# Kernel optimization log

Measured on AMD Instinct MI355X. Metric: run time of the kernel, lower is better.

The kernel has to match this reference:

```python
import jax, jax.numpy as jnp
import numpy as np

B, PP, LP, H = 128, 1024, 128, 256  # graphs, protein atoms/graph, ligand atoms/graph, hidden
NP, NL = B * PP, B * LP


def setup_inputs() -> dict:
    key = jax.random.key(0)
    ks = jax.random.split(key, 16)
    s = 0.02
    return {
        "protein_pos": 10.0 * jax.random.normal(ks[0], (NP, 3), jnp.float32),
        "ligand_pos": 10.0 * jax.random.normal(ks[1], (NL, 3), jnp.float32),
        "protein_element": jax.random.randint(ks[2], (NP,), 0, 128),
        "protein_aa": jax.random.randint(ks[3], (NP,), 0, 32),
        "protein_is_backbone": jax.random.randint(ks[4], (NP,), 0, 2),
        "ligand_type": jax.random.randint(ks[5], (NL,), 0, 16),
        "protein_batch": jnp.repeat(jnp.arange(B), PP),  # block-contiguous segments
        "ligand_batch": jnp.repeat(jnp.arange(B), LP),
        "E_elem": s * jax.random.normal(ks[6], (128, H), jnp.float32),
        "E_aa": s * jax.random.normal(ks[7], (32, H), jnp.float32),
        "E_bb": s * jax.random.normal(ks[8], (2, H), jnp.float32),
        "E_lig": s * jax.random.normal(ks[9], (16, H), jnp.float32),
        "Wd1": s * jax.random.normal(ks[10], (H, H), jnp.float32),
        "bd1": jnp.zeros((H,), jnp.float32),
        "Wd2": s * jax.random.normal(ks[11], (H, H), jnp.float32),
        "bd2": jnp.zeros((H,), jnp.float32),
        "Wa1": s * jax.random.normal(ks[12], (2 * H + 2, H), jnp.float32),
        "ba1": jnp.zeros((H,), jnp.float32),
        "Wa2": s * jax.random.normal(ks[13], (H, 1), jnp.float32),
        "ba2": jnp.zeros((1,), jnp.float32),
    }


def _pool_by_batch(x, batch, bsz):
    # mean-pool rows of x into bsz segments (index_add_ + bincount in torch)
    summed = jax.ops.segment_sum(x, batch, num_segments=bsz)
    counts = jax.ops.segment_sum(jnp.ones((x.shape[0],), x.dtype), batch, num_segments=bsz)
    return summed / jnp.maximum(counts, 1.0)[:, None]


def reference(protein_pos, ligand_pos, protein_element, protein_aa, protein_is_backbone,
              ligand_type, protein_batch, ligand_batch,
              E_elem, E_aa, E_bb, E_lig, Wd1, bd1, Wd2, bd2, Wa1, ba1, Wa2, ba2):
    # protein / ligand node embeddings
    h_protein = E_elem[protein_element] + E_aa[protein_aa] + E_bb[protein_is_backbone]
    h_ligand = E_lig[ligand_type]

    # compose_context: protein first, then ligand (mask_ligand = [0]*NP + [1]*NL)
    h_ctx = jnp.concatenate([h_protein, h_ligand], axis=0)

    # stub denoiser: pointwise 2-layer SiLU MLP producing out['h']
    h_out = jax.nn.silu(h_ctx @ Wd1 + bd1) @ Wd2 + bd2
    protein_h = h_out[:protein_pos.shape[0]]
    ligand_h = h_out[protein_pos.shape[0]:]

    pooled_protein = _pool_by_batch(protein_h, protein_batch, B)  # [B, H]
    pooled_ligand = _pool_by_batch(ligand_h, ligand_batch, B)     # [B, H]

    # contact features: per-graph cdist(lig, prot), min over protein atoms,
    # then mean & min over ligand atoms. Uniform block layout -> dense reshape.
    prot = protein_pos.reshape(B, PP, 3)
    lig = ligand_pos.reshape(B, LP, 3)
    d2 = jnp.sum((lig[:, :, None, :] - prot[:, None, :, :]) ** 2, axis=-1)  # [B, LP, PP]
    dist = jnp.sqrt(d2)
    min_lp = dist.min(axis=2)                                    # [B, LP]
    contact = jnp.stack([min_lp.mean(axis=1), min_lp.min(axis=1)], axis=-1)  # [B, 2]

    graph_feat = jnp.concatenate([pooled_protein, pooled_ligand, contact], axis=-1)  # [B, 2H+2]
    affinity = (jax.nn.silu(graph_feat @ Wa1 + ba1) @ Wa2 + ba2).squeeze(-1)  # [B]
    return affinity
```

## Files before the change

### kernel.cpp

```cpp
#include <hip/hip_runtime.h>
#include <hip/hip_bf16.h>

typedef _Float16 f16;
typedef _Float16 h4 __attribute__((ext_vector_type(4)));
typedef float f32x4 __attribute__((ext_vector_type(4)));

#define B_   128
#define PP_  1024
#define LP_  128
#define H_   256
#define NP_  131072
#define NL_  16384


__global__ void __launch_bounds__(256) prep_k(
    const float* __restrict__ W1,
    const float* __restrict__ Ee, const float* __restrict__ Ea,
    const float* __restrict__ Eb, const float* __restrict__ El,
    const float* __restrict__ bd1, const float* __restrict__ W2,
    const float* __restrict__ Wa1, const float* __restrict__ ba1,
    const float* __restrict__ bd2,
    f16* __restrict__ tbl, float* __restrict__ wc, float* __restrict__ cvec,
    float* __restrict__ ysum)
{
  __shared__ float src[256];
  const int bid = blockIdx.x, tid = threadIdx.x;
  if (bid < 256) ysum[bid * 256 + tid] = 0.f;

  if (bid < 178) {
    const float* s;
    float badd = 0.f;
    if (bid < 128)      s = Ee + bid * 256;
    else if (bid < 160) s = Ea + (bid - 128) * 256;
    else if (bid < 162) { s = Eb + (bid - 160) * 256; badd = bd1[tid]; }
    else                { s = El + (bid - 162) * 256; badd = bd1[tid]; }
    src[tid] = s[tid];
    __syncthreads();
    float a0 = 0.f, a1 = 0.f, a2 = 0.f, a3 = 0.f;
#pragma unroll 4
    for (int k = 0; k < 256; k += 4) {
      a0 += src[k]     * W1[(k)     * 256 + tid];
      a1 += src[k + 1] * W1[(k + 1) * 256 + tid];
      a2 += src[k + 2] * W1[(k + 2) * 256 + tid];
      a3 += src[k + 3] * W1[(k + 3) * 256 + tid];
    }
    tbl[bid * 256 + tid] = (f16)(((a0 + a1) + (a2 + a3)) + badd);
  } else if (bid < 690) {
    const int r = bid - 178;
    const int half = r >> 8, rr = r & 255;
    src[tid] = W2[rr * 256 + tid];
    __syncthreads();
    const float* W = Wa1 + half * 256 * 256 + tid;
    float a0 = 0.f, a1 = 0.f, a2 = 0.f, a3 = 0.f;
#pragma unroll 4
    for (int n = 0; n < 256; n += 4) {
      a0 += src[n]     * W[(n)     * 256];
      a1 += src[n + 1] * W[(n + 1) * 256];
      a2 += src[n + 2] * W[(n + 2) * 256];
      a3 += src[n + 3] * W[(n + 3) * 256];
    }
    const float scale = half ? (1.f / (float)LP_) : (1.f / (float)PP_);
    wc[half * 65536 + rr * 256 + tid] = ((a0 + a1) + (a2 + a3)) * scale;
  } else {
    float a = ba1[tid];
#pragma unroll 8
    for (int n = 0; n < 256; ++n)
      a += bd2[n] * (Wa1[n * 256 + tid] + Wa1[(256 + n) * 256 + tid]);
    cvec[tid] = a;
  }
}

__global__ void __launch_bounds__(256, 4) gpool_k(
    const int* __restrict__ pel, const int* __restrict__ paa,
    const int* __restrict__ pbb, const int* __restrict__ ltyp,
    const f16* __restrict__ tbl, float* __restrict__ ysum)
{
  const int tid = threadIdx.x, wave = tid >> 6, lane = tid & 63;
  const int batch = blockIdx.x / 18, g = blockIdx.x % 18;
  const int c0 = lane * 4;
  f32x4 acc = (f32x4){0.f, 0.f, 0.f, 0.f};

  if (g < 16) {
    const int base = batch * PP_ + g * 64 + wave * 16;
#pragma unroll 4
    for (int r = 0; r < 16; ++r) {
      const int idx = base + r;
      h4 va = *(const h4*)(tbl + pel[idx] * 256 + c0);
      h4 vb = *(const h4*)(tbl + 32768 + paa[idx] * 256 + c0);
      h4 vc = *(const h4*)(tbl + 40960 + pbb[idx] * 256 + c0);
#pragma unroll
      for (int i = 0; i < 4; ++i) {
        float pre = (float)va[i] + (float)vb[i] + (float)vc[i];
        acc[i] += pre * __builtin_amdgcn_rcpf(1.f + __expf(-pre));
      }
    }
  } else {
    const int base = batch * LP_ + (g - 16) * 64 + wave * 16;
#pragma unroll 4
    for (int r = 0; r < 16; ++r) {
      const int idx = base + r;
      h4 v = *(const h4*)(tbl + 41472 + ltyp[idx] * 256 + c0);
#pragma unroll
      for (int i = 0; i < 4; ++i) {
        float pre = (float)v[i];
        acc[i] += pre * __builtin_amdgcn_rcpf(1.f + __expf(-pre));
      }
    }
  }

  __shared__ f32x4 red[3][64];
  if (wave) red[wave - 1][lane] = acc;
  __syncthreads();
  if (wave == 0) {
    f32x4 a1 = red[0][lane], a2 = red[1][lane], a3 = red[2][lane];
    float* pool = ysum + (g < 16 ? 0 : 32768) + batch * 256 + c0;
#pragma unroll
    for (int i = 0; i < 4; ++i)
      atomicAdd(pool + i, ((acc[i] + a1[i]) + (a2[i] + a3[i])));
  }
}

__global__ void __launch_bounds__(512) head_k(
    const float* __restrict__ ppos, const float* __restrict__ lpos,
    const float* __restrict__ ysum, const float* __restrict__ wc,
    const float* __restrict__ cvec, const float* __restrict__ Wa1,
    const float* __restrict__ Wa2, const float* __restrict__ ba2,
    float* __restrict__ out)
{
  __shared__ float px[4 * 264], py[4 * 264], pz[4 * 264];
  __shared__ float ysc[512];
  __shared__ float part[512];
  __shared__ float lmin[128];
  __shared__ float cls[2];
  __shared__ float red[4];
  const int b = blockIdx.x, tid = threadIdx.x;

#pragma unroll
  for (int r = 0; r < 2; ++r) {
    const int i = r * 512 + tid;
    const int d = (i >> 8) * 264 + (i & 255);
    const float* p = ppos + ((size_t)b * PP_ + i) * 3;
    px[d] = p[0]; py[d] = p[1]; pz[d] = p[2];
  }
  ysc[tid] = (tid < 256) ? ysum[b * 256 + tid]
                         : ysum[32768 + b * 256 + (tid - 256)];
  __syncthreads();

  {
    const int lig = tid >> 2, prt = tid & 3;
    const float* lp = lpos + ((size_t)b * LP_ + lig) * 3;
    const float lx = lp[0], ly = lp[1], lz = lp[2];
    const float4* X4 = (const float4*)(px + prt * 264);
    const float4* Y4 = (const float4*)(py + prt * 264);
    const float4* Z4 = (const float4*)(pz + prt * 264);
    float m = 3.4e38f;
#pragma unroll 4
    for (int i = 0; i < 64; ++i) {
      float4 X = X4[i], Y = Y4[i], Z = Z4[i];
      float dx, dy, dz, d2;
      dx = lx - X.x; dy = ly - Y.x; dz = lz - Z.x;
      d2 = dx * dx + dy * dy + dz * dz; m = fminf(m, d2);
      dx = lx - X.y; dy = ly - Y.y; dz = lz - Z.y;
      d2 = dx * dx + dy * dy + dz * dz; m = fminf(m, d2);
      dx = lx - X.z; dy = ly - Y.z; dz = lz - Z.z;
      d2 = dx * dx + dy * dy + dz * dz; m = fminf(m, d2);
      dx = lx - X.w; dy = ly - Y.w; dz = lz - Z.w;
      d2 = dx * dx + dy * dy + dz * dz; m = fminf(m, d2);
    }
    m = fminf(m, __shfl_xor(m, 1));
    m = fminf(m, __shfl_xor(m, 2));
    if (prt == 0) lmin[lig] = sqrtf(m);
  }
  __syncthreads();
  if (tid < 64) {
    const float a0 = lmin[tid], a1 = lmin[tid + 64];
    float sm = a0 + a1, mn = fminf(a0, a1);
#pragma unroll
    for (int off = 32; off; off >>= 1) {
      sm += __shfl_down(sm, off);
      mn = fminf(mn, __shfl_down(mn, off));
    }
    if (tid == 0) { cls[0] = sm * (1.f / (float)LP_); cls[1] = mn; }
  }

  {
    const int gg = tid >> 8, j = tid & 255;
    const float* W = wc + gg * 65536 + j;
    const float* ys = ysc + gg * 256;
    float a[8];
#pragma unroll
    for (int u = 0; u < 8; ++u) a[u] = 0.f;
#pragma unroll 2
    for (int k = 0; k < 256; k += 8) {
#pragma unroll
      for (int u = 0; u < 8; ++u)
        a[u] += ys[k + u] * W[(k + u) * 256];
    }
    part[tid] = ((a[0] + a[1]) + (a[2] + a[3])) + ((a[4] + a[5]) + (a[6] + a[7]));
  }
  __syncthreads();

  if (tid < 256) {
    float pre = part[tid] + part[256 + tid] + cvec[tid]
              + cls[0] * Wa1[512 * 256 + tid] + cls[1] * Wa1[513 * 256 + tid];
    float si = pre * __builtin_amdgcn_rcpf(1.f + __expf(-pre));
    float p = si * Wa2[tid];
#pragma unroll
    for (int off = 32; off; off >>= 1) p += __shfl_down(p, off);
    if ((tid & 63) == 0) red[tid >> 6] = p;
  }
  __syncthreads();
  if (tid == 0) out[b] = (red[0] + red[1]) + (red[2] + red[3]) + ba2[0];
}

extern "C" void kernel_launch(void* const* d_in, const int* in_sizes, int n_in,
                              void* d_out, int out_size, void* d_ws, size_t ws_size,
                              hipStream_t stream)
{
  const float* protein_pos = (const float*)d_in[0];
  const float* ligand_pos  = (const float*)d_in[1];
  const int*   pel  = (const int*)d_in[2];
  const int*   paa  = (const int*)d_in[3];
  const int*   pbb  = (const int*)d_in[4];
  const int*   ltyp = (const int*)d_in[5];
  const float* Ee  = (const float*)d_in[8];
  const float* Ea  = (const float*)d_in[9];
  const float* Eb  = (const float*)d_in[10];
  const float* El  = (const float*)d_in[11];
  const float* Wd1 = (const float*)d_in[12];
  const float* bd1 = (const float*)d_in[13];
  const float* Wd2 = (const float*)d_in[14];
  const float* bd2 = (const float*)d_in[15];
  const float* Wa1 = (const float*)d_in[16];
  const float* ba1 = (const float*)d_in[17];
  const float* Wa2 = (const float*)d_in[18];
  const float* ba2 = (const float*)d_in[19];
  float* out = (float*)d_out;

  char* ws = (char*)d_ws;
  f16*   tbl  = (f16*)(ws);
  float* ysum = (float*)(ws + 98304);
  float* wc   = (float*)(ws + 360448);
  float* cvec = (float*)(ws + 884736);

  prep_k<<<691, 256, 0, stream>>>(Wd1, Ee, Ea, Eb, El, bd1, Wd2, Wa1, ba1, bd2,
                                  tbl, wc, cvec, ysum);
  gpool_k<<<B_ * 18, 256, 0, stream>>>(pel, paa, pbb, ltyp, tbl, ysum);
  head_k<<<B_, 512, 0, stream>>>(protein_pos, ligand_pos, ysum, wc, cvec,
                                 Wa1, Wa2, ba2, out);
}
```

Before: 139.9 us.

## Fuse prep, gather-pool and head kernels into one cooperative persistent kernel

Replaces three kernel launches with a single cooperative kernel of 512 blocks that uses grid-wide syncs between the weight-folding, gather/SiLU pooling and per-graph head phases. The pooling work is redistributed across the persistent grid and the per-block shared-memory reduction is dropped in favor of per-wave atomics. The head phase now runs with 256 threads per graph instead of 512, doing both matvec halves per thread. The aim is to remove launch gaps and inter-kernel idle time. In exchange it adds grid-sync overhead, more atomic traffic, and less parallelism in the head phase, where only 128 of the 512 blocks do work.

```diff
diff --git a/kernel.cpp b/kernel.cpp
--- a/kernel.cpp
+++ b/kernel.cpp
@@ -1,5 +1,8 @@
 #include <hip/hip_runtime.h>
+#include <hip/hip_cooperative_groups.h>
 #include <hip/hip_bf16.h>
+
+namespace cg = cooperative_groups;
 
 typedef _Float16 f16;
 typedef _Float16 h4 __attribute__((ext_vector_type(4)));
@@ -9,166 +12,171 @@
 #define PP_  1024
 #define LP_  128
 #define H_   256
-#define NP_  131072
-#define NL_  16384
-
-
-__global__ void __launch_bounds__(256) prep_k(
-    const float* __restrict__ W1,
+#define GRID_ 512
+
+
+__global__ void __launch_bounds__(256, 2) fused_k(
+    const int* __restrict__ pel, const int* __restrict__ paa,
+    const int* __restrict__ pbb, const int* __restrict__ ltyp,
+    const float* __restrict__ ppos, const float* __restrict__ lpos,
     const float* __restrict__ Ee, const float* __restrict__ Ea,
     const float* __restrict__ Eb, const float* __restrict__ El,
-    const float* __restrict__ bd1, const float* __restrict__ W2,
-    const float* __restrict__ Wa1, const float* __restrict__ ba1,
-    const float* __restrict__ bd2,
-    f16* __restrict__ tbl, float* __restrict__ wc, float* __restrict__ cvec,
-    float* __restrict__ ysum)
-{
-  __shared__ float src[256];
-  const int bid = blockIdx.x, tid = threadIdx.x;
-  if (bid < 256) ysum[bid * 256 + tid] = 0.f;
-
-  if (bid < 178) {
-    const float* s;
-    float badd = 0.f;
-    if (bid < 128)      s = Ee + bid * 256;
-    else if (bid < 160) s = Ea + (bid - 128) * 256;
-    else if (bid < 162) { s = Eb + (bid - 160) * 256; badd = bd1[tid]; }
-    else                { s = El + (bid - 162) * 256; badd = bd1[tid]; }
-    src[tid] = s[tid];
-    __syncthreads();
-    float a0 = 0.f, a1 = 0.f, a2 = 0.f, a3 = 0.f;
-#pragma unroll 4
-    for (int k = 0; k < 256; k += 4) {
-      a0 += src[k]     * W1[(k)     * 256 + tid];
-      a1 += src[k + 1] * W1[(k + 1) * 256 + tid];
-      a2 += src[k + 2] * W1[(k + 2) * 256 + tid];
-      a3 += src[k + 3] * W1[(k + 3) * 256 + tid];
-    }
-    tbl[bid * 256 + tid] = (f16)(((a0 + a1) + (a2 + a3)) + badd);
-  } else if (bid < 690) {
-    const int r = bid - 178;
-    const int half = r >> 8, rr = r & 255;
-    src[tid] = W2[rr * 256 + tid];
-    __syncthreads();
-    const float* W = Wa1 + half * 256 * 256 + tid;
-    float a0 = 0.f, a1 = 0.f, a2 = 0.f, a3 = 0.f;
-#pragma unroll 4
-    for (int n = 0; n < 256; n += 4) {
-      a0 += src[n]     * W[(n)     * 256];
-      a1 += src[n + 1] * W[(n + 1) * 256];
-      a2 += src[n + 2] * W[(n + 2) * 256];
-      a3 += src[n + 3] * W[(n + 3) * 256];
-    }
-    const float scale = half ? (1.f / (float)LP_) : (1.f / (float)PP_);
-    wc[half * 65536 + rr * 256 + tid] = ((a0 + a1) + (a2 + a3)) * scale;
-  } else {
-    float a = ba1[tid];
-#pragma unroll 8
-    for (int n = 0; n < 256; ++n)
-      a += bd2[n] * (Wa1[n * 256 + tid] + Wa1[(256 + n) * 256 + tid]);
-    cvec[tid] = a;
-  }
-}
-
-__global__ void __launch_bounds__(256, 4) gpool_k(
-    const int* __restrict__ pel, const int* __restrict__ paa,
-    const int* __restrict__ pbb, const int* __restrict__ ltyp,
-    const f16* __restrict__ tbl, float* __restrict__ ysum)
-{
-  const int tid = threadIdx.x, wave = tid >> 6, lane = tid & 63;
-  const int batch = blockIdx.x / 18, g = blockIdx.x % 18;
-  const int c0 = lane * 4;
-  f32x4 acc = (f32x4){0.f, 0.f, 0.f, 0.f};
-
-  if (g < 16) {
-    const int base = batch * PP_ + g * 64 + wave * 16;
-#pragma unroll 4
-    for (int r = 0; r < 16; ++r) {
-      const int idx = base + r;
-      h4 va = *(const h4*)(tbl + pel[idx] * 256 + c0);
-      h4 vb = *(const h4*)(tbl + 32768 + paa[idx] * 256 + c0);
-      h4 vc = *(const h4*)(tbl + 40960 + pbb[idx] * 256 + c0);
-#pragma unroll
-      for (int i = 0; i < 4; ++i) {
-        float pre = (float)va[i] + (float)vb[i] + (float)vc[i];
-        acc[i] += pre * __builtin_amdgcn_rcpf(1.f + __expf(-pre));
-      }
-    }
-  } else {
-    const int base = batch * LP_ + (g - 16) * 64 + wave * 16;
-#pragma unroll 4
-    for (int r = 0; r < 16; ++r) {
-      const int idx = base + r;
-      h4 v = *(const h4*)(tbl + 41472 + ltyp[idx] * 256 + c0);
-#pragma unroll
-      for (int i = 0; i < 4; ++i) {
-        float pre = (float)v[i];
-        acc[i] += pre * __builtin_amdgcn_rcpf(1.f + __expf(-pre));
-      }
-    }
-  }
-
-  __shared__ f32x4 red[3][64];
-  if (wave) red[wave - 1][lane] = acc;
-  __syncthreads();
-  if (wave == 0) {
-    f32x4 a1 = red[0][lane], a2 = red[1][lane], a3 = red[2][lane];
-    float* pool = ysum + (g < 16 ? 0 : 32768) + batch * 256 + c0;
-#pragma unroll
-    for (int i = 0; i < 4; ++i)
-      atomicAdd(pool + i, ((acc[i] + a1[i]) + (a2[i] + a3[i])));
-  }
-}
-
-__global__ void __launch_bounds__(512) head_k(
-    const float* __restrict__ ppos, const float* __restrict__ lpos,
-    const float* __restrict__ ysum, const float* __restrict__ wc,
-    const float* __restrict__ cvec, const float* __restrict__ Wa1,
+    const float* __restrict__ W1, const float* __restrict__ bd1,
+    const float* __restrict__ W2, const float* __restrict__ Wa1,
+    const float* __restrict__ ba1, const float* __restrict__ bd2,
     const float* __restrict__ Wa2, const float* __restrict__ ba2,
+    f16* __restrict__ tbl, float* __restrict__ wc,
+    float* __restrict__ cvec, float* __restrict__ ysum,
     float* __restrict__ out)
 {
+  cg::grid_group grid = cg::this_grid();
+  const int bid = blockIdx.x, tid = threadIdx.x;
+  const int wave = tid >> 6, lane = tid & 63;
+
+  __shared__ float src[256];
   __shared__ float px[4 * 264], py[4 * 264], pz[4 * 264];
+  __shared__ float lmin[128];
   __shared__ float ysc[512];
-  __shared__ float part[512];
-  __shared__ float lmin[128];
   __shared__ float cls[2];
   __shared__ float red[4];
-  const int b = blockIdx.x, tid = threadIdx.x;
-
-#pragma unroll
-  for (int r = 0; r < 2; ++r) {
-    const int i = r * 512 + tid;
+
+  if (bid < 256) ysum[bid * 256 + tid] = 0.f;
+
+#pragma unroll 1
+  for (int jj = 0; jj < 2; ++jj) {
+    const int j = bid + jj * GRID_;
+    if (j >= 691) break;
+    if (jj) __syncthreads();
+    if (j < 178) {
+      const float* s;
+      float badd = 0.f;
+      if (j < 128)      s = Ee + j * 256;
+      else if (j < 160) s = Ea + (j - 128) * 256;
+      else if (j < 162) { s = Eb + (j - 160) * 256; badd = bd1[tid]; }
+      else              { s = El + (j - 162) * 256; badd = bd1[tid]; }
+      src[tid] = s[tid];
+      __syncthreads();
+      float a0 = 0.f, a1 = 0.f, a2 = 0.f, a3 = 0.f;
+#pragma unroll 4
+      for (int k = 0; k < 256; k += 4) {
+        a0 += src[k]     * W1[(k)     * 256 + tid];
+        a1 += src[k + 1] * W1[(k + 1) * 256 + tid];
+        a2 += src[k + 2] * W1[(k + 2) * 256 + tid];
+        a3 += src[k + 3] * W1[(k + 3) * 256 + tid];
+      }
+      tbl[j * 256 + tid] = (f16)(((a0 + a1) + (a2 + a3)) + badd);
+    } else if (j < 690) {
+      const int r = j - 178;
+      const int half = r >> 8, rr = r & 255;
+      src[tid] = W2[rr * 256 + tid];
+      __syncthreads();
+      const float* W = Wa1 + half * 256 * 256 + tid;
+      float a0 = 0.f, a1 = 0.f, a2 = 0.f, a3 = 0.f;
+#pragma unroll 4
+      for (int n = 0; n < 256; n += 4) {
+        a0 += src[n]     * W[(n)     * 256];
+        a1 += src[n + 1] * W[(n + 1) * 256];
+        a2 += src[n + 2] * W[(n + 2) * 256];
+        a3 += src[n + 3] * W[(n + 3) * 256];
+      }
+      const float scale = half ? (1.f / (float)LP_) : (1.f / (float)PP_);
+      wc[half * 65536 + rr * 256 + tid] = ((a0 + a1) + (a2 + a3)) * scale;
+    } else {
+      float a = ba1[tid];
+#pragma unroll 8
+      for (int n = 0; n < 256; ++n)
+        a += bd2[n] * (Wa1[n * 256 + tid] + Wa1[(256 + n) * 256 + tid]);
+      cvec[tid] = a;
+    }
+  }
+
+  grid.sync();
+
+  {
+    const int c0 = lane * 4;
+#pragma unroll 1
+    for (int k = 0; k < 4; ++k) {
+      const int pj = bid + k * GRID_;
+      const int batch = pj >> 4, g = pj & 15;
+      const int base = batch * PP_ + g * 64 + wave * 16;
+      f32x4 acc = (f32x4){0.f, 0.f, 0.f, 0.f};
+#pragma unroll 4
+      for (int r = 0; r < 16; ++r) {
+        const int idx = base + r;
+        h4 va = *(const h4*)(tbl + pel[idx] * 256 + c0);
+        h4 vb = *(const h4*)(tbl + 32768 + paa[idx] * 256 + c0);
+        h4 vc = *(const h4*)(tbl + 40960 + pbb[idx] * 256 + c0);
+        h4 s = va + vb + vc;
+#pragma unroll
+        for (int i = 0; i < 4; ++i) {
+          float pre = (float)s[i];
+          acc[i] += pre * __builtin_amdgcn_rcpf(1.f + __expf(-pre));
+        }
+      }
+      float* pool = ysum + batch * 256 + c0;
+#pragma unroll
+      for (int i = 0; i < 4; ++i) atomicAdd(pool + i, acc[i]);
+    }
+    {
+      const int batch = bid >> 2, lg = bid & 3;
+      const int base = batch * LP_ + lg * 32 + wave * 8;
+      f32x4 acc = (f32x4){0.f, 0.f, 0.f, 0.f};
+#pragma unroll 4
+      for (int r = 0; r < 8; ++r) {
+        h4 v = *(const h4*)(tbl + 41472 + ltyp[base + r] * 256 + c0);
+#pragma unroll
+        for (int i = 0; i < 4; ++i) {
+          float pre = (float)v[i];
+          acc[i] += pre * __builtin_amdgcn_rcpf(1.f + __expf(-pre));
+        }
+      }
+      float* pool = ysum + 32768 + batch * 256 + c0;
+#pragma unroll
+      for (int i = 0; i < 4; ++i) atomicAdd(pool + i, acc[i]);
+    }
+  }
+
+  grid.sync();
+
+  if (bid >= B_) return;
+  const int b = bid;
+
+#pragma unroll
+  for (int r = 0; r < 4; ++r) {
+    const int i = r * 256 + tid;
     const int d = (i >> 8) * 264 + (i & 255);
     const float* p = ppos + ((size_t)b * PP_ + i) * 3;
     px[d] = p[0]; py[d] = p[1]; pz[d] = p[2];
   }
-  ysc[tid] = (tid < 256) ? ysum[b * 256 + tid]
-                         : ysum[32768 + b * 256 + (tid - 256)];
-  __syncthreads();
-
-  {
-    const int lig = tid >> 2, prt = tid & 3;
+  ysc[tid] = ysum[b * 256 + tid];
+  ysc[256 + tid] = ysum[32768 + b * 256 + tid];
+  __syncthreads();
+
+  {
+    const int lig = tid >> 1, prt = tid & 1;
     const float* lp = lpos + ((size_t)b * LP_ + lig) * 3;
     const float lx = lp[0], ly = lp[1], lz = lp[2];
-    const float4* X4 = (const float4*)(px + prt * 264);
-    const float4* Y4 = (const float4*)(py + prt * 264);
-    const float4* Z4 = (const float4*)(pz + prt * 264);
     float m = 3.4e38f;
-#pragma unroll 4
-    for (int i = 0; i < 64; ++i) {
-      float4 X = X4[i], Y = Y4[i], Z = Z4[i];
-      float dx, dy, dz, d2;
-      dx = lx - X.x; dy = ly - Y.x; dz = lz - Z.x;
-      d2 = dx * dx + dy * dy + dz * dz; m = fminf(m, d2);
-      dx = lx - X.y; dy = ly - Y.y; dz = lz - Z.y;
-      d2 = dx * dx + dy * dy + dz * dz; m = fminf(m, d2);
-      dx = lx - X.z; dy = ly - Y.z; dz = lz - Z.z;
-      d2 = dx * dx + dy * dy + dz * dz; m = fminf(m, d2);
-      dx = lx - X.w; dy = ly - Y.w; dz = lz - Z.w;
-      d2 = dx * dx + dy * dy + dz * dz; m = fminf(m, d2);
+#pragma unroll 1
+    for (int s2 = prt * 2; s2 < prt * 2 + 2; ++s2) {
+      const float4* X4 = (const float4*)(px + s2 * 264);
+      const float4* Y4 = (const float4*)(py + s2 * 264);
+      const float4* Z4 = (const float4*)(pz + s2 * 264);
+#pragma unroll 4
+      for (int i = 0; i < 64; ++i) {
+        float4 X = X4[i], Y = Y4[i], Z = Z4[i];
+        float dx, dy, dz, d2;
+        dx = lx - X.x; dy = ly - Y.x; dz = lz - Z.x;
+        d2 = dx * dx + dy * dy + dz * dz; m = fminf(m, d2);
+        dx = lx - X.y; dy = ly - Y.y; dz = lz - Z.y;
+        d2 = dx * dx + dy * dy + dz * dz; m = fminf(m, d2);
+        dx = lx - X.z; dy = ly - Y.z; dz = lz - Z.z;
+        d2 = dx * dx + dy * dy + dz * dz; m = fminf(m, d2);
+        dx = lx - X.w; dy = ly - Y.w; dz = lz - Z.w;
+        d2 = dx * dx + dy * dy + dz * dz; m = fminf(m, d2);
+      }
     }
     m = fminf(m, __shfl_xor(m, 1));
-    m = fminf(m, __shfl_xor(m, 2));
     if (prt == 0) lmin[lig] = sqrtf(m);
   }
   __syncthreads();
@@ -183,10 +191,9 @@
     if (tid == 0) { cls[0] = sm * (1.f / (float)LP_); cls[1] = mn; }
   }
 
-  {
-    const int gg = tid >> 8, j = tid & 255;
-    const float* W = wc + gg * 65536 + j;
-    const float* ys = ysc + gg * 256;
+  float mv;
+  {
+    const int j = tid;
     float a[8];
 #pragma unroll
     for (int u = 0; u < 8; ++u) a[u] = 0.f;
@@ -194,14 +201,20 @@
     for (int k = 0; k < 256; k += 8) {
 #pragma unroll
       for (int u = 0; u < 8; ++u)
-        a[u] += ys[k + u] * W[(k + u) * 256];
-    }
-    part[tid] = ((a[0] + a[1]) + (a[2] + a[3])) + ((a[4] + a[5]) + (a[6] + a[7]));
-  }
-  __syncthreads();
-
-  if (tid < 256) {
-    float pre = part[tid] + part[256 + tid] + cvec[tid]
+        a[u] += ysc[k + u] * wc[(k + u) * 256 + j];
+    }
+#pragma unroll 2
+    for (int k = 0; k < 256; k += 8) {
+#pragma unroll
+      for (int u = 0; u < 8; ++u)
+        a[u] += ysc[256 + k + u] * wc[65536 + (k + u) * 256 + j];
+    }
+    mv = ((a[0] + a[1]) + (a[2] + a[3])) + ((a[4] + a[5]) + (a[6] + a[7]));
+  }
+  __syncthreads();
+
+  {
+    float pre = mv + cvec[tid]
               + cls[0] * Wa1[512 * 256 + tid] + cls[1] * Wa1[513 * 256 + tid];
     float si = pre * __builtin_amdgcn_rcpf(1.f + __expf(-pre));
     float p = si * Wa2[tid];
@@ -243,9 +256,14 @@
   float* wc   = (float*)(ws + 360448);
   float* cvec = (float*)(ws + 884736);
 
-  prep_k<<<691, 256, 0, stream>>>(Wd1, Ee, Ea, Eb, El, bd1, Wd2, Wa1, ba1, bd2,
-                                  tbl, wc, cvec, ysum);
-  gpool_k<<<B_ * 18, 256, 0, stream>>>(pel, paa, pbb, ltyp, tbl, ysum);
-  head_k<<<B_, 512, 0, stream>>>(protein_pos, ligand_pos, ysum, wc, cvec,
-                                 Wa1, Wa2, ba2, out);
+  void* args[] = {
+    (void*)&pel, (void*)&paa, (void*)&pbb, (void*)&ltyp,
+    (void*)&protein_pos, (void*)&ligand_pos,
+    (void*)&Ee, (void*)&Ea, (void*)&Eb, (void*)&El,
+    (void*)&Wd1, (void*)&bd1, (void*)&Wd2, (void*)&Wa1,
+    (void*)&ba1, (void*)&bd2, (void*)&Wa2, (void*)&ba2,
+    (void*)&tbl, (void*)&wc, (void*)&cvec, (void*)&ysum, (void*)&out
+  };
+  hipLaunchCooperativeKernel((const void*)fused_k, dim3(GRID_), dim3(256),
+                             args, 0, stream);
 }
```

Result: slower. 325.3 us (+132.4%).

## Fuse pooling with head MLP and move contact distances into prep kernel

Applied to the files above, without the earlier changes.

Drops the precomputed W2·Wa1 folded weight matrix and bias vector, and applies W2 then Wa1 per graph inside a fused pooling+head kernel of one 1024-thread block per graph. The ligand-protein min-distance computation moves into the prep kernel as extra blocks alongside the embedding-table projection. This removes one launch, the atomic pooling buffer and its zeroing, and the large weight-fold matmul. In exchange, pooling parallelism falls to 128 blocks and each graph does two GEMVs.

```diff
diff --git a/kernel.cpp b/kernel.cpp
--- a/kernel.cpp
+++ b/kernel.cpp
@@ -2,30 +2,26 @@
 #include <hip/hip_bf16.h>
 
 typedef _Float16 f16;
-typedef _Float16 h4 __attribute__((ext_vector_type(4)));
-typedef float f32x4 __attribute__((ext_vector_type(4)));
+typedef _Float16 h2 __attribute__((ext_vector_type(2)));
 
 #define B_   128
 #define PP_  1024
 #define LP_  128
 #define H_   256
-#define NP_  131072
-#define NL_  16384
 
 
 __global__ void __launch_bounds__(256) prep_k(
     const float* __restrict__ W1,
     const float* __restrict__ Ee, const float* __restrict__ Ea,
     const float* __restrict__ Eb, const float* __restrict__ El,
-    const float* __restrict__ bd1, const float* __restrict__ W2,
-    const float* __restrict__ Wa1, const float* __restrict__ ba1,
-    const float* __restrict__ bd2,
-    f16* __restrict__ tbl, float* __restrict__ wc, float* __restrict__ cvec,
-    float* __restrict__ ysum)
+    const float* __restrict__ bd1,
+    const float* __restrict__ ppos, const float* __restrict__ lpos,
+    f16* __restrict__ tbl, float* __restrict__ cbuf)
 {
+  __shared__ float px[4 * 264], py[4 * 264], pz[4 * 264];
+  __shared__ float lmin[128];
   __shared__ float src[256];
   const int bid = blockIdx.x, tid = threadIdx.x;
-  if (bid < 256) ysum[bid * 256 + tid] = 0.f;
 
   if (bid < 178) {
     const float* s;
@@ -45,164 +41,157 @@
       a3 += src[k + 3] * W1[(k + 3) * 256 + tid];
     }
     tbl[bid * 256 + tid] = (f16)(((a0 + a1) + (a2 + a3)) + badd);
-  } else if (bid < 690) {
-    const int r = bid - 178;
-    const int half = r >> 8, rr = r & 255;
-    src[tid] = W2[rr * 256 + tid];
-    __syncthreads();
-    const float* W = Wa1 + half * 256 * 256 + tid;
-    float a0 = 0.f, a1 = 0.f, a2 = 0.f, a3 = 0.f;
-#pragma unroll 4
-    for (int n = 0; n < 256; n += 4) {
-      a0 += src[n]     * W[(n)     * 256];
-      a1 += src[n + 1] * W[(n + 1) * 256];
-      a2 += src[n + 2] * W[(n + 2) * 256];
-      a3 += src[n + 3] * W[(n + 3) * 256];
-    }
-    const float scale = half ? (1.f / (float)LP_) : (1.f / (float)PP_);
-    wc[half * 65536 + rr * 256 + tid] = ((a0 + a1) + (a2 + a3)) * scale;
-  } else {
-    float a = ba1[tid];
-#pragma unroll 8
-    for (int n = 0; n < 256; ++n)
-      a += bd2[n] * (Wa1[n * 256 + tid] + Wa1[(256 + n) * 256 + tid]);
-    cvec[tid] = a;
+    return;
+  }
+
+  const int b = bid - 178;
+#pragma unroll
+  for (int r = 0; r < 4; ++r) {
+    const int i = r * 256 + tid;
+    const int d = (i >> 8) * 264 + (i & 255);
+    const float* p = ppos + ((size_t)b * PP_ + i) * 3;
+    px[d] = p[0]; py[d] = p[1]; pz[d] = p[2];
+  }
+  __syncthreads();
+  {
+    const int lig = tid >> 1, prt = tid & 1;
+    const float* lp = lpos + ((size_t)b * LP_ + lig) * 3;
+    const float lx = lp[0], ly = lp[1], lz = lp[2];
+    float m = 3.4e38f;
+#pragma unroll 1
+    for (int s2 = prt * 2; s2 < prt * 2 + 2; ++s2) {
+      const float4* X4 = (const float4*)(px + s2 * 264);
+      const float4* Y4 = (const float4*)(py + s2 * 264);
+      const float4* Z4 = (const float4*)(pz + s2 * 264);
+#pragma unroll 4
+      for (int i = 0; i < 64; ++i) {
+        float4 X = X4[i], Y = Y4[i], Z = Z4[i];
+        float dx, dy, dz, d2;
+        dx = lx - X.x; dy = ly - Y.x; dz = lz - Z.x;
+        d2 = dx * dx + dy * dy + dz * dz; m = fminf(m, d2);
+        dx = lx - X.y; dy = ly - Y.y; dz = lz - Z.y;
+        d2 = dx * dx + dy * dy + dz * dz; m = fminf(m, d2);
+        dx = lx - X.z; dy = ly - Y.z; dz = lz - Z.z;
+        d2 = dx * dx + dy * dy + dz * dz; m = fminf(m, d2);
+        dx = lx - X.w; dy = ly - Y.w; dz = lz - Z.w;
+        d2 = dx * dx + dy * dy + dz * dz; m = fminf(m, d2);
+      }
+    }
+    m = fminf(m, __shfl_xor(m, 1));
+    if (prt == 0) lmin[lig] = sqrtf(m);
+  }
+  __syncthreads();
+  if (tid < 64) {
+    const float a0 = lmin[tid], a1 = lmin[tid + 64];
+    float sm = a0 + a1, mn = fminf(a0, a1);
+#pragma unroll
+    for (int off = 32; off; off >>= 1) {
+      sm += __shfl_down(sm, off);
+      mn = fminf(mn, __shfl_down(mn, off));
+    }
+    if (tid == 0) {
+      cbuf[b * 2 + 0] = sm * (1.f / (float)LP_);
+      cbuf[b * 2 + 1] = mn;
+    }
   }
 }
 
-__global__ void __launch_bounds__(256, 4) gpool_k(
+__global__ void __launch_bounds__(1024) pool_head_k(
     const int* __restrict__ pel, const int* __restrict__ paa,
     const int* __restrict__ pbb, const int* __restrict__ ltyp,
-    const f16* __restrict__ tbl, float* __restrict__ ysum)
-{
-  const int tid = threadIdx.x, wave = tid >> 6, lane = tid & 63;
-  const int batch = blockIdx.x / 18, g = blockIdx.x % 18;
-  const int c0 = lane * 4;
-  f32x4 acc = (f32x4){0.f, 0.f, 0.f, 0.f};
-
-  if (g < 16) {
-    const int base = batch * PP_ + g * 64 + wave * 16;
-#pragma unroll 4
-    for (int r = 0; r < 16; ++r) {
-      const int idx = base + r;
-      h4 va = *(const h4*)(tbl + pel[idx] * 256 + c0);
-      h4 vb = *(const h4*)(tbl + 32768 + paa[idx] * 256 + c0);
-      h4 vc = *(const h4*)(tbl + 40960 + pbb[idx] * 256 + c0);
-#pragma unroll
-      for (int i = 0; i < 4; ++i) {
-        float pre = (float)va[i] + (float)vb[i] + (float)vc[i];
-        acc[i] += pre * __builtin_amdgcn_rcpf(1.f + __expf(-pre));
-      }
-    }
-  } else {
-    const int base = batch * LP_ + (g - 16) * 64 + wave * 16;
-#pragma unroll 4
-    for (int r = 0; r < 16; ++r) {
-      const int idx = base + r;
-      h4 v = *(const h4*)(tbl + 41472 + ltyp[idx] * 256 + c0);
-#pragma unroll
-      for (int i = 0; i < 4; ++i) {
-        float pre = (float)v[i];
-        acc[i] += pre * __builtin_amdgcn_rcpf(1.f + __expf(-pre));
-      }
-    }
-  }
-
-  __shared__ f32x4 red[3][64];
-  if (wave) red[wave - 1][lane] = acc;
-  __syncthreads();
-  if (wave == 0) {
-    f32x4 a1 = red[0][lane], a2 = red[1][lane], a3 = red[2][lane];
-    float* pool = ysum + (g < 16 ? 0 : 32768) + batch * 256 + c0;
-#pragma unroll
-    for (int i = 0; i < 4; ++i)
-      atomicAdd(pool + i, ((acc[i] + a1[i]) + (a2[i] + a3[i])));
-  }
-}
-
-__global__ void __launch_bounds__(512) head_k(
-    const float* __restrict__ ppos, const float* __restrict__ lpos,
-    const float* __restrict__ ysum, const float* __restrict__ wc,
-    const float* __restrict__ cvec, const float* __restrict__ Wa1,
+    const f16* __restrict__ tbl, const float* __restrict__ cbuf,
+    const float* __restrict__ W2, const float* __restrict__ bd2,
+    const float* __restrict__ Wa1, const float* __restrict__ ba1,
     const float* __restrict__ Wa2, const float* __restrict__ ba2,
     float* __restrict__ out)
 {
-  __shared__ float px[4 * 264], py[4 * 264], pz[4 * 264];
-  __shared__ float ysc[512];
+  __shared__ float redP[8][256];
+  __shared__ float redL[8][256];
+  __shared__ float ys[512];
+  __shared__ float pooled[512];
   __shared__ float part[512];
-  __shared__ float lmin[128];
-  __shared__ float cls[2];
   __shared__ float red[4];
   const int b = blockIdx.x, tid = threadIdx.x;
-
-#pragma unroll
-  for (int r = 0; r < 2; ++r) {
-    const int i = r * 512 + tid;
-    const int d = (i >> 8) * 264 + (i & 255);
-    const float* p = ppos + ((size_t)b * PP_ + i) * 3;
-    px[d] = p[0]; py[d] = p[1]; pz[d] = p[2];
-  }
-  ysc[tid] = (tid < 256) ? ysum[b * 256 + tid]
-                         : ysum[32768 + b * 256 + (tid - 256)];
-  __syncthreads();
-
+  const int c2 = tid & 127;
+  const int rg = tid >> 7;
+
+  float aP0 = 0.f, aP1 = 0.f, aL0 = 0.f, aL1 = 0.f;
   {
-    const int lig = tid >> 2, prt = tid & 3;
-    const float* lp = lpos + ((size_t)b * LP_ + lig) * 3;
-    const float lx = lp[0], ly = lp[1], lz = lp[2];
-    const float4* X4 = (const float4*)(px + prt * 264);
-    const float4* Y4 = (const float4*)(py + prt * 264);
-    const float4* Z4 = (const float4*)(pz + prt * 264);
-    float m = 3.4e38f;
-#pragma unroll 4
-    for (int i = 0; i < 64; ++i) {
-      float4 X = X4[i], Y = Y4[i], Z = Z4[i];
-      float dx, dy, dz, d2;
-      dx = lx - X.x; dy = ly - Y.x; dz = lz - Z.x;
-      d2 = dx * dx + dy * dy + dz * dz; m = fminf(m, d2);
-      dx = lx - X.y; dy = ly - Y.y; dz = lz - Z.y;
-      d2 = dx * dx + dy * dy + dz * dz; m = fminf(m, d2);
-      dx = lx - X.z; dy = ly - Y.z; dz = lz - Z.z;
-      d2 = dx * dx + dy * dy + dz * dz; m = fminf(m, d2);
-      dx = lx - X.w; dy = ly - Y.w; dz = lz - Z.w;
-      d2 = dx * dx + dy * dy + dz * dz; m = fminf(m, d2);
-    }
-    m = fminf(m, __shfl_xor(m, 1));
-    m = fminf(m, __shfl_xor(m, 2));
-    if (prt == 0) lmin[lig] = sqrtf(m);
-  }
-  __syncthreads();
-  if (tid < 64) {
-    const float a0 = lmin[tid], a1 = lmin[tid + 64];
-    float sm = a0 + a1, mn = fminf(a0, a1);
-#pragma unroll
-    for (int off = 32; off; off >>= 1) {
-      sm += __shfl_down(sm, off);
-      mn = fminf(mn, __shfl_down(mn, off));
-    }
-    if (tid == 0) { cls[0] = sm * (1.f / (float)LP_); cls[1] = mn; }
-  }
-
-  {
-    const int gg = tid >> 8, j = tid & 255;
-    const float* W = wc + gg * 65536 + j;
-    const float* ys = ysc + gg * 256;
-    float a[8];
-#pragma unroll
-    for (int u = 0; u < 8; ++u) a[u] = 0.f;
-#pragma unroll 2
-    for (int k = 0; k < 256; k += 8) {
-#pragma unroll
-      for (int u = 0; u < 8; ++u)
-        a[u] += ys[k + u] * W[(k + u) * 256];
-    }
-    part[tid] = ((a[0] + a[1]) + (a[2] + a[3])) + ((a[4] + a[5]) + (a[6] + a[7]));
+    const int pbase = b * PP_ + rg * 128;
+#pragma unroll 4
+    for (int r = 0; r < 128; ++r) {
+      const int idx = pbase + r;
+      h2 va = *(const h2*)(tbl + pel[idx] * 256 + c2 * 2);
+      h2 vb = *(const h2*)(tbl + 32768 + paa[idx] * 256 + c2 * 2);
+      h2 vc = *(const h2*)(tbl + 40960 + pbb[idx] * 256 + c2 * 2);
+      h2 s = va + vb + vc;
+      float p0 = (float)s[0], p1 = (float)s[1];
+      aP0 += p0 * __builtin_amdgcn_rcpf(1.f + __expf(-p0));
+      aP1 += p1 * __builtin_amdgcn_rcpf(1.f + __expf(-p1));
+    }
+    const int lbase = b * LP_ + rg * 16;
+#pragma unroll 4
+    for (int r = 0; r < 16; ++r) {
+      h2 v = *(const h2*)(tbl + 41472 + ltyp[lbase + r] * 256 + c2 * 2);
+      float p0 = (float)v[0], p1 = (float)v[1];
+      aL0 += p0 * __builtin_amdgcn_rcpf(1.f + __expf(-p0));
+      aL1 += p1 * __builtin_amdgcn_rcpf(1.f + __expf(-p1));
+    }
+  }
+  redP[rg][c2 * 2] = aP0; redP[rg][c2 * 2 + 1] = aP1;
+  redL[rg][c2 * 2] = aL0; redL[rg][c2 * 2 + 1] = aL1;
+  __syncthreads();
+
+  if (tid < 512) {
+    const int h = tid >> 8, c = tid & 255;
+    float s = 0.f;
+    if (h == 0) {
+#pragma unroll
+      for (int g = 0; g < 8; ++g) s += redP[g][c];
+    } else {
+#pragma unroll
+      for (int g = 0; g < 8; ++g) s += redL[g][c];
+    }
+    ys[h * 256 + c] = s;
+  }
+  __syncthreads();
+
+  if (tid < 512) {
+    const int h = tid >> 8, n = tid & 255;
+    const float* y = ys + h * 256;
+    float a0 = 0.f, a1 = 0.f, a2 = 0.f, a3 = 0.f;
+#pragma unroll 4
+    for (int k = 0; k < 256; k += 4) {
+      a0 += y[k]     * W2[(k)     * 256 + n];
+      a1 += y[k + 1] * W2[(k + 1) * 256 + n];
+      a2 += y[k + 2] * W2[(k + 2) * 256 + n];
+      a3 += y[k + 3] * W2[(k + 3) * 256 + n];
+    }
+    const float scale = h ? (1.f / (float)LP_) : (1.f / (float)PP_);
+    pooled[tid] = ((a0 + a1) + (a2 + a3)) * scale + bd2[n];
+  }
+  __syncthreads();
+
+  if (tid < 512) {
+    const int kh = tid >> 8, j = tid & 255;
+    const float* W = Wa1 + kh * 256 * 256 + j;
+    const float* p = pooled + kh * 256;
+    float a0 = 0.f, a1 = 0.f, a2 = 0.f, a3 = 0.f;
+#pragma unroll 4
+    for (int n = 0; n < 256; n += 4) {
+      a0 += p[n]     * W[(n)     * 256];
+      a1 += p[n + 1] * W[(n + 1) * 256];
+      a2 += p[n + 2] * W[(n + 2) * 256];
+      a3 += p[n + 3] * W[(n + 3) * 256];
+    }
+    part[tid] = (a0 + a1) + (a2 + a3);
   }
   __syncthreads();
 
   if (tid < 256) {
-    float pre = part[tid] + part[256 + tid] + cvec[tid]
-              + cls[0] * Wa1[512 * 256 + tid] + cls[1] * Wa1[513 * 256 + tid];
+    const float c0 = cbuf[b * 2], c1 = cbuf[b * 2 + 1];
+    float pre = part[tid] + part[256 + tid] + ba1[tid]
+              + c0 * Wa1[512 * 256 + tid] + c1 * Wa1[513 * 256 + tid];
     float si = pre * __builtin_amdgcn_rcpf(1.f + __expf(-pre));
     float p = si * Wa2[tid];
 #pragma unroll
@@ -239,13 +228,10 @@
 
   char* ws = (char*)d_ws;
   f16*   tbl  = (f16*)(ws);
-  float* ysum = (float*)(ws + 98304);
-  float* wc   = (float*)(ws + 360448);
-  float* cvec = (float*)(ws + 884736);
-
-  prep_k<<<691, 256, 0, stream>>>(Wd1, Ee, Ea, Eb, El, bd1, Wd2, Wa1, ba1, bd2,
-                                  tbl, wc, cvec, ysum);
-  gpool_k<<<B_ * 18, 256, 0, stream>>>(pel, paa, pbb, ltyp, tbl, ysum);
-  head_k<<<B_, 512, 0, stream>>>(protein_pos, ligand_pos, ysum, wc, cvec,
-                                 Wa1, Wa2, ba2, out);
+  float* cbuf = (float*)(ws + 98304);
+
+  prep_k<<<306, 256, 0, stream>>>(Wd1, Ee, Ea, Eb, El, bd1,
+                                  protein_pos, ligand_pos, tbl, cbuf);
+  pool_head_k<<<B_, 1024, 0, stream>>>(pel, paa, pbb, ltyp, tbl, cbuf,
+                                       Wd2, bd2, Wa1, ba1, Wa2, ba2, out);
 }
```

Result: slower. 150.8 us (+7.7%).
